# Optimization experiments

Measured on AMD Instinct MI355X. Metric: run time of the kernel, lower is better.

Reference implementation:

```python
import jax, jax.numpy as jnp
import numpy as np

N = 8192
F_IN = 128
D = 128
NEG_SLOPE = 0.2  # cfg.negativeslope (standard GAT value)
MASK_FILL = -9e15


def setup_inputs() -> dict:
    key = jax.random.key(0)
    k1, k2, k3, k4 = jax.random.split(key, 4)
    A = jax.random.randint(k1, (N, N), 0, 2, dtype=jnp.int32)
    X = jax.random.normal(k2, (N, F_IN), dtype=jnp.float32)
    # glorot init for Ws, xavier_uniform(gain=1.414) for a
    lim_w = float(np.sqrt(6.0 / (F_IN + D)))
    Ws = jax.random.uniform(k3, (F_IN, D), minval=-lim_w, maxval=lim_w, dtype=jnp.float32)
    lim_a = 1.414 * float(np.sqrt(6.0 / (2 * D + 1)))
    a = jax.random.uniform(k4, (2 * D, 1), minval=-lim_a, maxval=lim_a, dtype=jnp.float32)
    return {"A": A, "X": X, "Ws": Ws, "a": a}


def reference(A, X, Ws, a):
    # Wh: [N, D]
    Wh = X @ Ws
    d = Wh.shape[-1]
    # additive attention: e_ij = leaky_relu(Wh_i . a1 + Wh_j . a2)
    e1 = Wh @ a[:d]          # [N, 1]
    e2 = Wh @ a[d:]          # [N, 1]
    e = jax.nn.leaky_relu(e1 + e2.T, negative_slope=NEG_SLOPE)  # [N, N]
    e = jnp.where(A > 0, e, MASK_FILL)
    attn = jax.nn.softmax(e, axis=1)  # row-wise over neighbors
    H = attn @ Wh            # [N, D]
    return H
```

## Files before the change

### kernel.cpp

```cpp
#include <hip/hip_runtime.h>
#include <hip/hip_bf16.h>

#define NN 8192
#define DD 128

typedef __attribute__((ext_vector_type(8))) short short8;
typedef __attribute__((ext_vector_type(4))) float f32x4;
typedef unsigned int u32;
typedef unsigned long long u64;

__device__ __forceinline__ ushort f2bf(float f) {
    __hip_bfloat16 h = __float2bfloat16(f);
    return *(ushort*)&h;
}

__device__ __forceinline__ void async_ld16(const void* g, void* l) {
    __builtin_amdgcn_global_load_lds(
        (const __attribute__((address_space(1))) u32*)g,
        (__attribute__((address_space(3))) u32*)l, 16, 0, 0);
}

__global__ __launch_bounds__(256) void k12_gemm(const float* __restrict__ X,
                                                const float* __restrict__ Ws,
                                                const float* __restrict__ a,
                                                ushort* __restrict__ WhT,
                                                float* __restrict__ C1,
                                                float* __restrict__ C1s,
                                                float2* __restrict__ E2) {
    __shared__ float lWs[128 * 132];
    __shared__ float lX[32 * 132];
    __shared__ ushort lT2[128 * 32];
    __shared__ float la[256];
    int t = threadIdx.x, bx = blockIdx.x;
    la[t] = a[t];
    const float4* Ws4 = (const float4*)Ws;
    const float4* X4 = (const float4*)X;
    for (int j = 0; j < 16; ++j) {
        int u = j * 256 + t;
        int k = u >> 5, c4 = u & 31;
        *(float4*)&lWs[k * 132 + c4 * 4] = Ws4[u];
    }
    for (int j = 0; j < 4; ++j) {
        int u = j * 256 + t;
        int r = u >> 5, c4 = u & 31;
        *(float4*)&lX[r * 132 + c4 * 4] = X4[bx * 1024 + u];
    }
    __syncthreads();
    int r0 = (t >> 5) * 4, c0 = (t & 31) * 4;
    float acc[4][4];
#pragma unroll
    for (int i = 0; i < 4; ++i)
#pragma unroll
        for (int j = 0; j < 4; ++j) acc[i][j] = 0.f;
#pragma unroll 4
    for (int k = 0; k < 128; ++k) {
        float4 wv = *(const float4*)&lWs[k * 132 + c0];
        float x0 = lX[(r0 + 0) * 132 + k];
        float x1 = lX[(r0 + 1) * 132 + k];
        float x2 = lX[(r0 + 2) * 132 + k];
        float x3 = lX[(r0 + 3) * 132 + k];
#pragma unroll
        for (int j = 0; j < 4; ++j) {
            acc[0][j] += x0 * ((const float*)&wv)[j];
            acc[1][j] += x1 * ((const float*)&wv)[j];
            acc[2][j] += x2 * ((const float*)&wv)[j];
            acc[3][j] += x3 * ((const float*)&wv)[j];
        }
    }
#pragma unroll
    for (int i = 0; i < 4; ++i)
#pragma unroll
        for (int j = 0; j < 4; ++j)
            lT2[(c0 + j) * 32 + r0 + i] = f2bf(acc[i][j]);
    float p1[4], p2[4];
#pragma unroll
    for (int i = 0; i < 4; ++i) {
        p1[i] = 0.f; p2[i] = 0.f;
#pragma unroll
        for (int j = 0; j < 4; ++j) {
            p1[i] += acc[i][j] * la[c0 + j];
            p2[i] += acc[i][j] * la[128 + c0 + j];
        }
    }
#pragma unroll
    for (int m = 1; m < 32; m <<= 1) {
#pragma unroll
        for (int i = 0; i < 4; ++i) {
            p1[i] += __shfl_xor(p1[i], m);
            p2[i] += __shfl_xor(p2[i], m);
        }
    }
    if ((t & 31) == 0) {
#pragma unroll
        for (int i = 0; i < 4; ++i) {
            int row = bx * 32 + r0 + i;
            C1[row]  = __expf(p1[i]);
            C1s[row] = __expf(0.2f * p1[i]);
            E2[row]  = make_float2(__expf(p2[i]), __expf(0.2f * p2[i]));
        }
    }
    __syncthreads();
    {
        int d = t >> 1, hf = t & 1;
        uint4* dst = (uint4*)&WhT[(size_t)d * NN + bx * 32 + hf * 16];
        const uint4* src = (const uint4*)&lT2[d * 32 + hf * 16];
        dst[0] = src[0];
        dst[1] = src[1];
    }
}

#define MROW 72

__global__ __launch_bounds__(512, 2) void k3_main(
    const int* __restrict__ A, const ushort* __restrict__ WhT,
    const float* __restrict__ C1, const float* __restrict__ C1s,
    const float2* __restrict__ E2,
    float* __restrict__ Hp, float* __restrict__ Lp) {

    __shared__ __align__(16) char lB[131072];
    __shared__ __align__(16) char lE[4096];
    __shared__ __align__(16) char lM[256 * MROW];

    int tid = threadIdx.x;
    int lane = tid & 63;
    int w = tid >> 6;
    int n = lane & 15;
    int kg = lane >> 4;

    int bx = blockIdx.x;
    int kb = blockIdx.y;
    int rb = bx * 256 + w * 32;

    float c1_0 = C1[rb + n],      c1s_0 = C1s[rb + n];
    float c1_1 = C1[rb + 16 + n], c1s_1 = C1s[rb + 16 + n];

#pragma unroll
    for (int i = 0; i < 16; ++i) {
        int p = w + i * 8;
        int kt = p >> 4, tp = (p >> 3) & 1, c = p & 7;
        const ushort* src = WhT + (size_t)(c * 16 + n) * NN +
                            (size_t)kb * 512 + kt * 64 + tp * 32 + kg * 8;
        async_ld16(src, lB + p * 1024 + lane * 16);
    }
    if (w == 0)
#pragma unroll
        for (int i = 0; i < 4; ++i)
            async_ld16((const char*)(E2 + (size_t)kb * 512) + (i * 64 + lane) * 16,
                       lE + (i * 64 + lane) * 16);

    {
        const int* pA = A + (size_t)(rb) * NN + (size_t)kb * 512 + lane;
        for (int r8 = 0; r8 < 32; ++r8) {
            const int* rp = pA + (size_t)r8 * NN;
            int v[8];
#pragma unroll
            for (int c = 0; c < 8; ++c)
                v[c] = __builtin_nontemporal_load(rp + c * 64);
#pragma unroll
            for (int c = 0; c < 8; ++c) {
                u64 m = __ballot(v[c] != 0);
                if (lane == 0)
                    *(u64*)(lM + (w * 32 + r8) * MROW + c * 8) = m;
            }
        }
    }

    short8 ones;
#pragma unroll
    for (int j = 0; j < 8; ++j) ones[j] = (short)0x3F80;

    f32x4 acc0[8], acc1[8];
#pragma unroll
    for (int c = 0; c < 8; ++c) {
        acc0[c] = (f32x4){0.f, 0.f, 0.f, 0.f};
        acc1[c] = (f32x4){0.f, 0.f, 0.f, 0.f};
    }
    f32x4 accl0 = (f32x4){0.f, 0.f, 0.f, 0.f};
    f32x4 accl1 = (f32x4){0.f, 0.f, 0.f, 0.f};

    __syncthreads();

    const char* mrow0 = lM + (w * 32 + n) * MROW;
    const char* mrow1 = lM + (w * 32 + 16 + n) * MROW;

    for (int kt = 0; kt < 8; ++kt) {
        uint2 m0 = *(const uint2*)(mrow0 + kt * 8);
        uint2 m1 = *(const uint2*)(mrow1 + kt * 8);
#pragma unroll
        for (int tp = 0; tp < 2; ++tp) {
            const float4* ev = (const float4*)((const float*)lE +
                                               (kt * 64 + tp * 32 + kg * 8) * 2);
            float pe[16];
            *(float4*)(pe + 0)  = ev[0];
            *(float4*)(pe + 4)  = ev[1];
            *(float4*)(pe + 8)  = ev[2];
            *(float4*)(pe + 12) = ev[3];
            u32 ab0 = ((tp ? m0.y : m0.x) >> (kg * 8)) & 0xffu;
            u32 ab1 = ((tp ? m1.y : m1.x) >> (kg * 8)) & 0xffu;
            short8 af0, af1;
#pragma unroll
            for (int u = 0; u < 8; ++u) {
                float w0 = fmaxf(c1_0 * pe[2 * u], c1s_0 * pe[2 * u + 1]);
                float w1 = fmaxf(c1_1 * pe[2 * u], c1s_1 * pe[2 * u + 1]);
                af0[u] = ((ab0 >> u) & 1u) ? (short)f2bf(w0) : (short)0;
                af1[u] = ((ab1 >> u) & 1u) ? (short)f2bf(w1) : (short)0;
            }
            const short8* bb = (const short8*)(lB + (kt * 16 + tp * 8) * 1024);
#pragma unroll
            for (int c = 0; c < 8; ++c) {
                short8 bf = bb[c * 64 + lane];
                acc0[c] = __builtin_amdgcn_mfma_f32_16x16x32_bf16(af0, bf, acc0[c], 0, 0, 0);
                acc1[c] = __builtin_amdgcn_mfma_f32_16x16x32_bf16(af1, bf, acc1[c], 0, 0, 0);
            }
            accl0 = __builtin_amdgcn_mfma_f32_16x16x32_bf16(af0, ones, accl0, 0, 0, 0);
            accl1 = __builtin_amdgcn_mfma_f32_16x16x32_bf16(af1, ones, accl1, 0, 0, 0);
        }
    }

    float* Hpb = Hp + (size_t)kb * (NN * DD);
#pragma unroll
    for (int c = 0; c < 8; ++c)
#pragma unroll
        for (int r = 0; r < 4; ++r) {
            Hpb[(size_t)(rb + kg * 4 + r) * DD + c * 16 + n]      = acc0[c][r];
            Hpb[(size_t)(rb + 16 + kg * 4 + r) * DD + c * 16 + n] = acc1[c][r];
        }
    if (n == 0) {
        float* Lpb = Lp + (size_t)kb * NN;
#pragma unroll
        for (int r = 0; r < 4; ++r) {
            Lpb[rb + kg * 4 + r]      = accl0[r];
            Lpb[rb + 16 + kg * 4 + r] = accl1[r];
        }
    }
}

__global__ void k4_final(const float* __restrict__ Hp, const float* __restrict__ Lp,
                         float* __restrict__ out) {
    int g = blockIdx.x * 256 + threadIdx.x;
    int i = g >> 5;
    float4 sv = make_float4(0.f, 0.f, 0.f, 0.f);
    float l = 0.f;
#pragma unroll
    for (int kb = 0; kb < 16; ++kb) {
        float4 v = *(const float4*)(Hp + (size_t)kb * (NN * DD) + (size_t)g * 4);
        sv.x += v.x; sv.y += v.y; sv.z += v.z; sv.w += v.w;
        l += Lp[(size_t)kb * NN + i];
    }
    float r = 1.f / l;
    *(float4*)(out + (size_t)g * 4) = make_float4(sv.x * r, sv.y * r, sv.z * r, sv.w * r);
}

extern "C" void kernel_launch(void* const* d_in, const int* in_sizes, int n_in,
                              void* d_out, int out_size, void* d_ws, size_t ws_size,
                              hipStream_t stream) {
    const int*   A  = (const int*)d_in[0];
    const float* X  = (const float*)d_in[1];
    const float* Ws = (const float*)d_in[2];
    const float* a  = (const float*)d_in[3];
    float* out = (float*)d_out;

    char* ws = (char*)d_ws;
    ushort* WhT = (ushort*)(ws);
    float*  C1  = (float*)(ws + (2u << 20));
    float*  C1s = (float*)(ws + (2u << 20) + (32u << 10));
    float2* E2  = (float2*)(ws + (2u << 20) + (64u << 10));
    float*  Hp  = (float*)(ws + (3u << 20));
    float*  Lp  = (float*)(ws + (67u << 20));

    k12_gemm<<<256, 256, 0, stream>>>(X, Ws, a, WhT, C1, C1s, E2);
    k3_main<<<dim3(32, 16), 512, 0, stream>>>(A, WhT, C1, C1s, E2, Hp, Lp);
    k4_final<<<1024, 256, 0, stream>>>(Hp, Lp, out);
}
```

Measured before the change: 411.1 us.

## Pack adjacency matrix into bitmask in separate kernel before main attention kernel

Adds a pre-pass kernel that reads the int32 adjacency matrix with 16-byte vector loads and packs it into a per-row bitmask laid out in the exact order the main kernel consumes. The main kernel then loads its mask bits directly into registers, dropping the per-row ballot loop and the LDS mask buffer. The aim is to make the 256MB A read a wide, fully parallel streaming pass and to shorten the main kernel's prologue, which frees shared memory. The cost is an extra kernel launch and an 8MB workspace write and read.

```diff
diff --git a/kernel.cpp b/kernel.cpp
--- a/kernel.cpp
+++ b/kernel.cpp
@@ -6,6 +6,7 @@
 
 typedef __attribute__((ext_vector_type(8))) short short8;
 typedef __attribute__((ext_vector_type(4))) float f32x4;
+typedef __attribute__((ext_vector_type(4))) int i32x4;
 typedef unsigned int u32;
 typedef unsigned long long u64;
 
@@ -18,6 +19,42 @@
     __builtin_amdgcn_global_load_lds(
         (const __attribute__((address_space(1))) u32*)g,
         (__attribute__((address_space(3))) u32*)l, 16, 0, 0);
+}
+
+#define PACK4(b, v, sh)                                     \
+    b |= (u32)((v).x & 1) << (sh);                          \
+    b |= (u32)((v).y & 1) << ((sh) + 1);                    \
+    b |= (u32)((v).z & 1) << ((sh) + 2);                    \
+    b |= (u32)((v).w & 1) << ((sh) + 3);
+
+__global__ __launch_bounds__(256) void k3a_pack(const int* __restrict__ A,
+                                                uint4* __restrict__ Ap) {
+    u32 T = blockIdx.x * 256 + threadIdx.x;
+    u32 row = T >> 6, q = T & 63, kb = q >> 2, kg = q & 3;
+    const int* base = A + (size_t)row * NN + kb * 512 + kg * 8;
+    u32 d[4];
+#pragma unroll
+    for (int h = 0; h < 2; ++h) {
+        i32x4 v[16];
+#pragma unroll
+        for (int j = 0; j < 8; ++j) {
+            int kt = h * 4 + (j >> 1), tp = j & 1;
+            const int* p = base + kt * 64 + tp * 32;
+            v[j * 2]     = __builtin_nontemporal_load((const i32x4*)p);
+            v[j * 2 + 1] = __builtin_nontemporal_load((const i32x4*)(p + 4));
+        }
+        u32 b01 = 0, b23 = 0;
+#pragma unroll
+        for (int j = 0; j < 8; ++j) {
+            u32 b = 0;
+            PACK4(b, v[j * 2], 0);
+            PACK4(b, v[j * 2 + 1], 4);
+            if (j < 4) b01 |= b << (8 * j);
+            else       b23 |= b << (8 * (j - 4));
+        }
+        d[h * 2] = b01; d[h * 2 + 1] = b23;
+    }
+    Ap[T] = make_uint4(d[0], d[1], d[2], d[3]);
 }
 
 __global__ __launch_bounds__(256) void k12_gemm(const float* __restrict__ X,
@@ -109,17 +146,14 @@
     }
 }
 
-#define MROW 72
-
-__global__ __launch_bounds__(512, 2) void k3_main(
-    const int* __restrict__ A, const ushort* __restrict__ WhT,
+__global__ __launch_bounds__(512, 2) void k3b_main(
+    const uint4* __restrict__ Ap, const ushort* __restrict__ WhT,
     const float* __restrict__ C1, const float* __restrict__ C1s,
     const float2* __restrict__ E2,
     float* __restrict__ Hp, float* __restrict__ Lp) {
 
     __shared__ __align__(16) char lB[131072];
     __shared__ __align__(16) char lE[4096];
-    __shared__ __align__(16) char lM[256 * MROW];
 
     int tid = threadIdx.x;
     int lane = tid & 63;
@@ -133,6 +167,9 @@
 
     float c1_0 = C1[rb + n],      c1s_0 = C1s[rb + n];
     float c1_1 = C1[rb + 16 + n], c1s_1 = C1s[rb + 16 + n];
+
+    uint4 Mq0 = Ap[(size_t)(rb + n) * 64 + kb * 4 + kg];
+    uint4 Mq1 = Ap[(size_t)(rb + 16 + n) * 64 + kb * 4 + kg];
 
 #pragma unroll
     for (int i = 0; i < 16; ++i) {
@@ -148,23 +185,6 @@
             async_ld16((const char*)(E2 + (size_t)kb * 512) + (i * 64 + lane) * 16,
                        lE + (i * 64 + lane) * 16);
 
-    {
-        const int* pA = A + (size_t)(rb) * NN + (size_t)kb * 512 + lane;
-        for (int r8 = 0; r8 < 32; ++r8) {
-            const int* rp = pA + (size_t)r8 * NN;
-            int v[8];
-#pragma unroll
-            for (int c = 0; c < 8; ++c)
-                v[c] = __builtin_nontemporal_load(rp + c * 64);
-#pragma unroll
-            for (int c = 0; c < 8; ++c) {
-                u64 m = __ballot(v[c] != 0);
-                if (lane == 0)
-                    *(u64*)(lM + (w * 32 + r8) * MROW + c * 8) = m;
-            }
-        }
-    }
-
     short8 ones;
 #pragma unroll
     for (int j = 0; j < 8; ++j) ones[j] = (short)0x3F80;
@@ -180,14 +200,16 @@
 
     __syncthreads();
 
-    const char* mrow0 = lM + (w * 32 + n) * MROW;
-    const char* mrow1 = lM + (w * 32 + 16 + n) * MROW;
-
+#pragma unroll
     for (int kt = 0; kt < 8; ++kt) {
-        uint2 m0 = *(const uint2*)(mrow0 + kt * 8);
-        uint2 m1 = *(const uint2*)(mrow1 + kt * 8);
 #pragma unroll
         for (int tp = 0; tp < 2; ++tp) {
+            const int j = kt * 2 + tp;
+            u32 d0 = (j < 4) ? Mq0.x : (j < 8) ? Mq0.y : (j < 12) ? Mq0.z : Mq0.w;
+            u32 d1 = (j < 4) ? Mq1.x : (j < 8) ? Mq1.y : (j < 12) ? Mq1.z : Mq1.w;
+            u32 ab0 = (d0 >> ((j & 3) * 8)) & 0xffu;
+            u32 ab1 = (d1 >> ((j & 3) * 8)) & 0xffu;
+
             const float4* ev = (const float4*)((const float*)lE +
                                                (kt * 64 + tp * 32 + kg * 8) * 2);
             float pe[16];
@@ -195,8 +217,6 @@
             *(float4*)(pe + 4)  = ev[1];
             *(float4*)(pe + 8)  = ev[2];
             *(float4*)(pe + 12) = ev[3];
-            u32 ab0 = ((tp ? m0.y : m0.x) >> (kg * 8)) & 0xffu;
-            u32 ab1 = ((tp ? m1.y : m1.x) >> (kg * 8)) & 0xffu;
             short8 af0, af1;
 #pragma unroll
             for (int u = 0; u < 8; ++u) {
@@ -261,14 +281,16 @@
     float* out = (float*)d_out;
 
     char* ws = (char*)d_ws;
-    ushort* WhT = (ushort*)(ws);
-    float*  C1  = (float*)(ws + (2u << 20));
-    float*  C1s = (float*)(ws + (2u << 20) + (32u << 10));
-    float2* E2  = (float2*)(ws + (2u << 20) + (64u << 10));
-    float*  Hp  = (float*)(ws + (3u << 20));
-    float*  Lp  = (float*)(ws + (67u << 20));
-
+    uint4*  Ap  = (uint4*)(ws);
+    ushort* WhT = (ushort*)(ws + (8u << 20));
+    float*  C1  = (float*)(ws + (10u << 20));
+    float*  C1s = (float*)(ws + (10u << 20) + (32u << 10));
+    float2* E2  = (float2*)(ws + (10u << 20) + (64u << 10));
+    float*  Hp  = (float*)(ws + (11u << 20));
+    float*  Lp  = (float*)(ws + (75u << 20));
+
+    k3a_pack<<<2048, 256, 0, stream>>>(A, Ap);
     k12_gemm<<<256, 256, 0, stream>>>(X, Ws, a, WhT, C1, C1s, E2);
-    k3_main<<<dim3(32, 16), 512, 0, stream>>>(A, WhT, C1, C1s, E2, Hp, Lp);
+    k3b_main<<<dim3(32, 16), 512, 0, stream>>>(Ap, WhT, C1, C1s, E2, Hp, Lp);
     k4_final<<<1024, 256, 0, stream>>>(Hp, Lp, out);
 }
```

Result: no change. 411.1 us (+0.0%).
